# Performance work log

Measured on AMD Instinct MI355X. Metric: run time of the kernel, lower is better.

Reference implementation:

```python
import jax, jax.numpy as jnp
import numpy as np

C = 256
G = 32  # GroupNorm groups
EPS = 1e-6


def setup_inputs() -> dict:
    key = jax.random.key(0)
    ks = jax.random.split(key, 11)
    B, H, W = 4, 64, 64
    scale = 0.02
    return {
        "x": jax.random.normal(ks[0], (B, C, H, W), dtype=jnp.float32),
        "gn_scale": jnp.ones((C,), jnp.float32),
        "gn_bias": jnp.zeros((C,), jnp.float32),
        "wq": jax.random.normal(ks[1], (C, C), jnp.float32) * scale,
        "bq": jnp.zeros((C,), jnp.float32),
        "wk": jax.random.normal(ks[2], (C, C), jnp.float32) * scale,
        "bk": jnp.zeros((C,), jnp.float32),
        "wv": jax.random.normal(ks[3], (C, C), jnp.float32) * scale,
        "bv": jnp.zeros((C,), jnp.float32),
        "wp": jax.random.normal(ks[4], (C, C), jnp.float32) * scale,
        "bp": jnp.zeros((C,), jnp.float32),
    }


def _group_norm(x, scale, bias):
    b, c, h, w = x.shape
    xr = x.reshape(b, G, c // G, h, w)
    mu = jnp.mean(xr, axis=(2, 3, 4), keepdims=True)
    var = jnp.var(xr, axis=(2, 3, 4), keepdims=True)
    xn = ((xr - mu) * jax.lax.rsqrt(var + EPS)).reshape(b, c, h, w)
    return xn * scale[None, :, None, None] + bias[None, :, None, None]


def _conv1x1(x, w, bch):
    # 1x1 conv == channel-mixing matmul; w is (out_ch, in_ch)
    return jnp.einsum('bchw,dc->bdhw', x, w) + bch[None, :, None, None]


def reference(x, gn_scale, gn_bias, wq, bq, wk, bk, wv, bv, wp, bp):
    b, c, h, w = x.shape
    hn = _group_norm(x, gn_scale, gn_bias)
    q = _conv1x1(hn, wq, bq).reshape(b, c, h * w)  # (b,c,N)
    k = _conv1x1(hn, wk, bk).reshape(b, c, h * w)
    v = _conv1x1(hn, wv, bv).reshape(b, c, h * w)
    # attn[b,i,j] = softmax_j( q_i . k_j / sqrt(c) )
    attn = jax.nn.softmax(jnp.einsum('bci,bcj->bij', q, k) * (c ** -0.5), axis=-1)
    A = jnp.einsum('bcj,bij->bci', v, attn).reshape(b, c, h, w)
    return x + _conv1x1(A, wp, bp)
```

## Files before the change

### kernel.cpp

```cpp
#include <hip/hip_runtime.h>
#include <stdint.h>

#define Bn 4
#define Cn 256
#define Gn 32
#define Nn 4096
#define CGn 8

typedef unsigned short u16;
typedef __attribute__((ext_vector_type(8))) short short8;
typedef __attribute__((ext_vector_type(4))) short short4v;
typedef __attribute__((ext_vector_type(4))) float f32x4;
typedef __attribute__((ext_vector_type(16))) float f32x16;

__device__ __forceinline__ u16 f2bf(float x) {
  uint32_t u = __float_as_uint(x);
  u += 0x7fffu + ((u >> 16) & 1u);
  return (u16)(u >> 16);
}
__device__ __forceinline__ float b2f(u16 v) {
  return __uint_as_float(((uint32_t)v) << 16);
}

__device__ __forceinline__ void gl_lds16(const void* g, void* l) {
  __builtin_amdgcn_global_load_lds(
      (__attribute__((address_space(1))) void*)(uintptr_t)g,
      (__attribute__((address_space(3))) void*)(uintptr_t)l, 16, 0, 0);
}

__device__ __forceinline__ int sw512(int row, int cb) { return row * 512 + ((cb ^ (row & 7)) * 16); }

__global__ void k_cs(const float* __restrict__ wq, const float* __restrict__ wk,
                     const float* __restrict__ wv, const float* __restrict__ wp,
                     const float* __restrict__ bq, const float* __restrict__ bk,
                     const float* __restrict__ bv, const float* __restrict__ x,
                     u16* __restrict__ wqkv, u16* __restrict__ wpb,
                     float* __restrict__ bqkv, float* __restrict__ stats) {
  if (blockIdx.x < 256) {
    const float s = 0.09016844005556021f;
    int i = blockIdx.x * 256 + threadIdx.x;
    wqkv[i]          = f2bf(wq[i] * s);
    wqkv[i + 65536]  = f2bf(wk[i]);
    wqkv[i + 131072] = f2bf(wv[i]);
    wpb[i]           = f2bf(wp[i]);
    if (i < 256) { bqkv[i] = bq[i] * s; bqkv[i + 256] = bk[i]; bqkv[i + 512] = bv[i]; }
  } else {
    int blk = blockIdx.x - 256;
    int grp = blk >> 2, part = blk & 3;
    const float4* base = (const float4*)(x + (size_t)grp * (CGn * Nn) + part * 8192);
    float s = 0.f, s2 = 0.f;
    for (int i = threadIdx.x; i < 2048; i += 256) {
      float4 v = base[i];
      s  += v.x + v.y + v.z + v.w;
      s2 += v.x * v.x + v.y * v.y + v.z * v.z + v.w * v.w;
    }
#pragma unroll
    for (int m = 1; m < 64; m <<= 1) { s += __shfl_xor(s, m, 64); s2 += __shfl_xor(s2, m, 64); }
    __shared__ float ps[4], ps2[4];
    int w = threadIdx.x >> 6;
    if ((threadIdx.x & 63) == 0) { ps[w] = s; ps2[w] = s2; }
    __syncthreads();
    if (threadIdx.x == 0) {
      stats[grp * 8 + part * 2]     = ps[0] + ps[1] + ps[2] + ps[3];
      stats[grp * 8 + part * 2 + 1] = ps2[0] + ps2[1] + ps2[2] + ps2[3];
    }
  }
}

__global__ void k_apply(const float* __restrict__ x, const float* __restrict__ stats,
                        const float* __restrict__ gsc, const float* __restrict__ gbi,
                        u16* __restrict__ hnT) {
  __shared__ __align__(16) char smem[32768];
  __shared__ float smu[Gn], srs[Gn];
  int n0 = blockIdx.x * 64;
  int b = blockIdx.y;
  int tid = threadIdx.x;
  if (tid < Gn) {
    float S = 0.f, S2 = 0.f;
#pragma unroll
    for (int p = 0; p < 4; ++p) {
      S  += stats[(b * Gn + tid) * 8 + p * 2];
      S2 += stats[(b * Gn + tid) * 8 + p * 2 + 1];
    }
    const float inv = 1.f / (CGn * Nn);
    float mu = S * inv;
    float var = S2 * inv - mu * mu;
    smu[tid] = mu;
    srs[tid] = rsqrtf(var + 1e-6f);
  }
  __syncthreads();
  int nl = (tid & 15) * 4;
  int cbase = tid >> 4;
  for (int pass = 0; pass < 16; ++pass) {
    int c = pass * 16 + cbase;
    float4 v = *(const float4*)(x + (size_t)b * Cn * Nn + (size_t)c * Nn + n0 + nl);
    int g = c >> 3;
    float sc = gsc[c] * srs[g];
    float bi = gbi[c] - smu[g] * sc;
    float vals[4] = {v.x, v.y, v.z, v.w};
#pragma unroll
    for (int i = 0; i < 4; ++i) {
      int row = nl + i;
      int off = row * 512 + ((((c >> 3) + row) & 31) * 16) + (c & 7) * 2;
      *(u16*)(smem + off) = f2bf(vals[i] * sc + bi);
    }
  }
  __syncthreads();
#pragma unroll
  for (int p = 0; p < 8; ++p) {
    int idx = p * 256 + tid;
    int row = idx >> 5, pc = idx & 31;
    int gc = (pc - row) & 31;
    short8 v8 = *(const short8*)(smem + row * 512 + pc * 16);
    *(short8*)(hnT + ((size_t)b * Nn + n0 + row) * Cn + gc * 8) = v8;
  }
}

__global__ __launch_bounds__(256, 2)
void k_qkv(const u16* __restrict__ wqkv, const float* __restrict__ bqkv,
           const u16* __restrict__ hnT, u16* __restrict__ qT, u16* __restrict__ kT,
           u16* __restrict__ vv) {
  __shared__ __align__(16) char smem[65536];
  const int tid = threadIdx.x, lane = tid & 63, w = tid >> 6;
  const int quad = (lane >> 4) & 3, low = lane & 15;
  const int d0 = blockIdx.y * 64, b = blockIdx.z;
  const int n_base = blockIdx.x * 256;
  const int which = d0 >> 8;
  const int dl0 = d0 & 255;
  const u16* hb = hnT + (size_t)b * Nn * Cn;
  const int scol = lane & 31;

#define QKV_STAGE(bsel, nt)                                                     \
  {                                                                             \
    _Pragma("unroll") for (int s = 0; s < 8; ++s) {                             \
      int r = w * 16 + s * 2 + (lane >> 5);                                     \
      int gc = (scol - r) & 31;                                                 \
      gl_lds16(hb + (size_t)(n_base + (nt) * 64 + r) * Cn + gc * 8,             \
               smem + (bsel) * 32768 + (w * 16 + s * 2) * 512);                 \
    }                                                                           \
  }

  QKV_STAGE(0, 0);
  short8 af[8];
  {
    const u16* wrow = wqkv + (size_t)(d0 + w * 16 + low) * Cn + quad * 8;
#pragma unroll
    for (int kk = 0; kk < 8; ++kk) af[kk] = *(const short8*)(wrow + kk * 32);
  }
  float bias[4];
#pragma unroll
  for (int r = 0; r < 4; ++r) bias[r] = bqkv[d0 + w * 16 + quad * 4 + r];

  for (int nt = 0; nt < 4; ++nt) {
    if (nt < 3) {
      QKV_STAGE((nt + 1) & 1, nt + 1);
      asm volatile("s_waitcnt vmcnt(10)" ::: "memory");
    } else {
      asm volatile("s_waitcnt vmcnt(0)" ::: "memory");
    }
    asm volatile("s_barrier" ::: "memory");
    char* buf = smem + (nt & 1) * 32768;
    f32x4 acc[4] = {{0.f,0.f,0.f,0.f},{0.f,0.f,0.f,0.f},{0.f,0.f,0.f,0.f},{0.f,0.f,0.f,0.f}};
#pragma unroll
    for (int kk = 0; kk < 8; ++kk)
#pragma unroll
      for (int t = 0; t < 4; ++t) {
        int row = t * 16 + low;
        short8 bf = *(const short8*)(buf + row * 512 + (((kk * 4 + quad) + row) & 31) * 16);
        acc[t] = __builtin_amdgcn_mfma_f32_16x16x32_bf16(af[kk], bf, acc[t], 0, 0, 0);
      }
    asm volatile("s_barrier" ::: "memory");
    char* Q = buf + w * 8192;
    if (which == 2) {
#pragma unroll
      for (int t = 0; t < 4; ++t)
#pragma unroll
        for (int r = 0; r < 4; ++r)
          *(u16*)(Q + (quad * 4 + r) * 144 + t * 32 + low * 2) = f2bf(acc[t][r] + bias[r]);
#pragma unroll
      for (int s = 0; s < 2; ++s) {
        int slot = s * 64 + lane;
        int row = slot >> 3, ch = slot & 7;
        short8 v8 = *(const short8*)(Q + row * 144 + ch * 16);
        *(short8*)(vv + (size_t)b * Cn * Nn + (size_t)(dl0 + w * 16 + row) * Nn +
                   n_base + nt * 64 + ch * 8) = v8;
      }
    } else {
#pragma unroll
      for (int t = 0; t < 4; ++t) {
        short4v pk;
#pragma unroll
        for (int r = 0; r < 4; ++r) pk[r] = (short)f2bf(acc[t][r] + bias[r]);
        *(short4v*)(Q + (t * 16 + low) * 48 + quad * 8) = pk;
      }
      u16* dst = (which == 0 ? qT : kT) + (size_t)b * Nn * Cn;
#pragma unroll
      for (int s = 0; s < 2; ++s) {
        int slot = s * 64 + lane;
        int row = slot >> 1, half = slot & 1;
        short8 v8 = *(const short8*)(Q + row * 48 + half * 16);
        *(short8*)(dst + (size_t)(n_base + nt * 64 + row) * Cn + dl0 + w * 16 + half * 8) = v8;
      }
    }
  }
#undef QKV_STAGE
}

__device__ __forceinline__ void flash_stage(char* smem, int bsel, const u16* kTb,
                                            const u16* vb, int j0, int w, int lo,
                                            int kr, int vr, int vp) {
  char* ksb = smem + bsel * 32768;
  char* vsb = ksb + 16384;
#pragma unroll
  for (int s = 0; s < 4; ++s) {
    int j = kr + s * 2;
    int gc = (lo - j) & 31;
    gl_lds16(kTb + (size_t)(j0 + j) * Cn + gc * 8, ksb + (w * 8 + s * 2) * 512);
  }
#pragma unroll
  for (int s = 0; s < 4; ++s) {
    int c = vr + s * 16;
    int gc = (vp - c - (c >> 2)) & 3;
    gl_lds16(vb + (size_t)c * Nn + j0 + gc * 8, vsb + (w * 64 + s * 16) * 64);
  }
}

__global__ __launch_bounds__(256, 2)
void k_flash(const u16* __restrict__ qT, const u16* __restrict__ kT,
             const u16* __restrict__ vv, u16* __restrict__ Op0,
             u16* __restrict__ Op1, u16* __restrict__ Op2, u16* __restrict__ Op3,
             float* __restrict__ lrow) {
  __shared__ __align__(16) char smem[65536];
  const int tid = threadIdx.x, lane = tid & 63, w = tid >> 6;
  const int lo = lane & 31, hi = lane >> 5;
  const int i0 = blockIdx.x * 128;
  const int b = blockIdx.y, jh = blockIdx.z;
  const u16* qTb = qT + (size_t)b * Nn * Cn;
  const u16* kTb = kT + (size_t)b * Nn * Cn;
  const u16* vb  = vv + (size_t)b * Cn * Nn;
  const int u7 = lo + hi;
  const int u9 = lo + hi + (lo >> 2);
  const int kr = w * 8 + hi;
  const int vr = w * 64 + (lane >> 2);
  const int vp = lane & 3;

  flash_stage(smem, 0, kTb, vb, jh * 1024, w, lo, kr, vr, vp);

  short8 qf[16];
  {
    const u16* qrow = qTb + (size_t)(i0 + w * 32 + lo) * Cn + hi * 8;
#pragma unroll
    for (int ks = 0; ks < 16; ++ks) qf[ks] = *(const short8*)(qrow + ks * 16);
  }
  f32x16 Oa[8];
#pragma unroll
  for (int ct = 0; ct < 8; ++ct)
#pragma unroll
    for (int e = 0; e < 16; ++e) Oa[ct][e] = 0.f;
  float l_ = 0.f;

  for (int jt = 0; jt < 32; ++jt) {
    if (jt < 31) {
      flash_stage(smem, (jt + 1) & 1, kTb, vb, jh * 1024 + (jt + 1) * 32, w, lo, kr, vr, vp);
      asm volatile("s_waitcnt vmcnt(8)" ::: "memory");
    } else {
      asm volatile("s_waitcnt vmcnt(0)" ::: "memory");
    }
    asm volatile("s_barrier" ::: "memory");
    const char* ksb = smem + (jt & 1) * 32768;
    const char* vsb = ksb + 16384;

    f32x16 S0;
#pragma unroll
    for (int e = 0; e < 16; ++e) S0[e] = 0.f;
#pragma unroll
    for (int ks = 0; ks < 16; ++ks) {
      int ch = (ks * 2 + u7) & 31;
      short8 a0 = *(const short8*)(ksb + lo * 512 + ch * 16);
      S0 = __builtin_amdgcn_mfma_f32_32x32x16_bf16(a0, qf[ks], S0, 0, 0, 0);
    }
    uint32_t Pp[8];
#pragma unroll
    for (int g = 0; g < 8; ++g) {
      float p0 = __builtin_amdgcn_exp2f(S0[2 * g]);
      float p1 = __builtin_amdgcn_exp2f(S0[2 * g + 1]);
      l_ += p0 + p1;
      Pp[g] = ((uint32_t)f2bf(p1) << 16) | f2bf(p0);
    }
#pragma unroll
    for (int kst = 0; kst < 2; ++kst) {
      uint32_t a0 = Pp[4 * kst], a1 = Pp[4 * kst + 1];
      uint32_t b0 = Pp[4 * kst + 2], b1 = Pp[4 * kst + 3];
      uint32_t s0 = hi ? a0 : b0, s1 = hi ? a1 : b1;
      uint32_t r0 = (uint32_t)__shfl_xor((int)s0, 32, 64);
      uint32_t r1 = (uint32_t)__shfl_xor((int)s1, 32, 64);
      union { uint32_t u[4]; short8 s8; } pu;
      pu.u[0] = hi ? r0 : a0;
      pu.u[1] = hi ? r1 : a1;
      pu.u[2] = hi ? b0 : r0;
      pu.u[3] = hi ? b1 : r1;
      int ch = (kst * 2 + u9) & 3;
#pragma unroll
      for (int ct = 0; ct < 8; ++ct) {
        short8 vf = *(const short8*)(vsb + (ct * 32 + lo) * 64 + ch * 16);
        Oa[ct] = __builtin_amdgcn_mfma_f32_32x32x16_bf16(vf, pu.s8, Oa[ct], 0, 0, 0);
      }
    }
    asm volatile("s_barrier" ::: "memory");
  }

  l_ += __shfl_xor(l_, 32, 64);
  if (hi == 0)
    lrow[(size_t)jh * (Bn * Nn) + (size_t)b * Nn + i0 + w * 32 + lo] = l_;
  float invl = __builtin_amdgcn_rcpf(l_);
  __syncthreads();
#pragma unroll
  for (int ct = 0; ct < 8; ++ct)
#pragma unroll
    for (int g = 0; g < 4; ++g) {
      short4v pk;
#pragma unroll
      for (int r = 0; r < 4; ++r) pk[r] = (short)f2bf(Oa[ct][g * 4 + r] * invl);
      int chv = (ct * 4 + g + lo) & 31;
      *(short4v*)(smem + w * 16384 + lo * 512 + chv * 16 + hi * 8) = pk;
    }
  __syncthreads();
  u16* Opj = (jh == 0) ? Op0 : (jh == 1) ? Op1 : (jh == 2) ? Op2 : Op3;
  u16* Ob = Opj + ((size_t)b * Nn + i0 + w * 32) * (size_t)Cn;
#pragma unroll
  for (int s = 0; s < 16; ++s) {
    int rr = s * 2 + hi;
    short8 v8 = *(const short8*)(smem + w * 16384 + rr * 512 + lo * 16);
    int gc = (lo - rr) & 31;
    *(short8*)(Ob + (size_t)rr * Cn + gc * 8) = v8;
  }
}

__global__ void k_comb(const u16* __restrict__ O0, const u16* __restrict__ O1,
                       const u16* __restrict__ O2, const u16* __restrict__ O3,
                       const float* __restrict__ lrow, u16* __restrict__ OT) {
  int gid = blockIdx.x * 256 + threadIdx.x;
  int row = gid >> 6;
  int c4 = (gid & 63) << 2;
  float L = lrow[row] + lrow[Bn * Nn + row] + lrow[2 * Bn * Nn + row] + lrow[3 * Bn * Nn + row];
  float inv = __builtin_amdgcn_rcpf(L);
  size_t base = (size_t)row * Cn + c4;
  short4v a0 = *(const short4v*)(O0 + base);
  short4v a1 = *(const short4v*)(O1 + base);
  short4v a2 = *(const short4v*)(O2 + base);
  short4v a3 = *(const short4v*)(O3 + base);
  short4v o;
#pragma unroll
  for (int i = 0; i < 4; ++i)
    o[i] = (short)f2bf((b2f((u16)a0[i]) + b2f((u16)a1[i]) + b2f((u16)a2[i]) + b2f((u16)a3[i])) * inv);
  *(short4v*)(OT + base) = o;
}

__global__ __launch_bounds__(256, 2)
void k_proj(const u16* __restrict__ wpb, const float* __restrict__ bp,
            const u16* __restrict__ OT, const float* __restrict__ x,
            float* __restrict__ out) {
  __shared__ __align__(16) char smem[65536];
  int tid = threadIdx.x, lane = tid & 63, w = tid >> 6, quad = lane >> 4, low = lane & 15;
  int n0 = blockIdx.x * 64, d0 = blockIdx.y * 64, b = blockIdx.z;
  {
    int r0 = w * 16;
#pragma unroll
    for (int s = 0; s < 8; ++s) {
      int rs = r0 + s * 2;
      int r = rs + (lane >> 5);
      int cb = (lane & 31) ^ (r & 7);
      gl_lds16(wpb + (size_t)(d0 + r) * Cn + cb * 8, smem + rs * 512);
      gl_lds16(OT + ((size_t)b * Nn + n0 + r) * Cn + cb * 8, smem + 32768 + rs * 512);
    }
  }
  asm volatile("s_waitcnt vmcnt(0)" ::: "memory");
  __syncthreads();
  f32x4 acc[4] = {{0.f,0.f,0.f,0.f},{0.f,0.f,0.f,0.f},{0.f,0.f,0.f,0.f},{0.f,0.f,0.f,0.f}};
#pragma unroll
  for (int kk = 0; kk < 8; ++kk) {
    short8 af = *(const short8*)(smem + sw512(w * 16 + low, kk * 4 + quad));
#pragma unroll
    for (int t = 0; t < 4; ++t) {
      short8 bf = *(const short8*)(smem + 32768 + sw512(t * 16 + low, kk * 4 + quad));
      acc[t] = __builtin_amdgcn_mfma_f32_16x16x32_bf16(af, bf, acc[t], 0, 0, 0);
    }
  }
  int dloc = d0 + w * 16 + quad * 4;
#pragma unroll
  for (int t = 0; t < 4; ++t)
#pragma unroll
    for (int r = 0; r < 4; ++r) {
      size_t idx = (size_t)b * Cn * Nn + (size_t)(dloc + r) * Nn + n0 + t * 16 + low;
      out[idx] = x[idx] + acc[t][r] + bp[dloc + r];
    }
}

extern "C" void kernel_launch(void* const* d_in, const int* in_sizes, int n_in,
                              void* d_out, int out_size, void* d_ws, size_t ws_size,
                              hipStream_t stream) {
  const float* x   = (const float*)d_in[0];
  const float* gsc = (const float*)d_in[1];
  const float* gbi = (const float*)d_in[2];
  const float* wq  = (const float*)d_in[3];
  const float* bq  = (const float*)d_in[4];
  const float* wk  = (const float*)d_in[5];
  const float* bk  = (const float*)d_in[6];
  const float* wv  = (const float*)d_in[7];
  const float* bv  = (const float*)d_in[8];
  const float* wp  = (const float*)d_in[9];
  const float* bp  = (const float*)d_in[10];
  float* out = (float*)d_out;

  char* ws = (char*)d_ws;
  u16*   wqkv  = (u16*)(ws + 0);
  u16*   wpb   = (u16*)(ws + 393216);
  float* bqkv  = (float*)(ws + 524288);
  float* stats = (float*)(ws + 527360);
  float* lrow  = (float*)(ws + 532480);
  u16*   hnT   = (u16*)(ws + 1048576);
  u16*   qT    = (u16*)(ws + 9437184);
  u16*   kT    = (u16*)(ws + 17825792);
  u16*   vv    = (u16*)(ws + 26214400);
  u16*   Op1   = (u16*)(ws + 34603008);
  u16*   Op2   = (u16*)(ws + 42991616);
  u16*   Op3   = (u16*)(ws + 51380224);

  k_cs<<<768, 256, 0, stream>>>(wq, wk, wv, wp, bq, bk, bv, x, wqkv, wpb, bqkv, stats);
  k_apply<<<dim3(64, 4), 256, 0, stream>>>(x, stats, gsc, gbi, hnT);
  k_qkv<<<dim3(16, 12, 4), 256, 0, stream>>>(wqkv, bqkv, hnT, qT, kT, vv);
  k_flash<<<dim3(32, 4, 4), 256, 0, stream>>>(qT, kT, vv, hnT , Op1, Op2, Op3, lrow);
  k_comb<<<4096, 256, 0, stream>>>(hnT, Op1, Op2, Op3, lrow, qT );
  k_proj<<<dim3(64, 4, 4), 256, 0, stream>>>(wpb, bp, qT , x, out);
}
```

Baseline: 200.9 us.

## Use hardware bf16 pack conversion, permlane32 swap, and MFMA priority hints

Replaces the software round-to-nearest-even bf16 conversion with the gfx950 v_cvt_pk_bf16_f32 instruction in the QKV projection, flash softmax and output epilogue. Replaces the shfl_xor-and-select exchange of P fragments between wave halves with v_permlane32_swap_b32. Wraps the MFMA loops in s_setprio raises so waves issuing matrix ops are favored during scheduling. The aim is to cut VALU and LDS-permute overhead in the attention inner loop; the priority hints may or may not help interleaving across waves.

```diff
diff --git a/kernel.cpp b/kernel.cpp
--- a/kernel.cpp
+++ b/kernel.cpp
@@ -175,8 +175,14 @@
 #pragma unroll
       for (int t = 0; t < 4; ++t)
 #pragma unroll
-        for (int r = 0; r < 4; ++r)
-          *(u16*)(Q + (quad * 4 + r) * 144 + t * 32 + low * 2) = f2bf(acc[t][r] + bias[r]);
+        for (int rp = 0; rp < 2; ++rp) {
+          uint32_t wv2;
+          float f0 = acc[t][2 * rp] + bias[2 * rp];
+          float f1 = acc[t][2 * rp + 1] + bias[2 * rp + 1];
+          asm("v_cvt_pk_bf16_f32 %0, %1, %2" : "=v"(wv2) : "v"(f0), "v"(f1));
+          *(u16*)(Q + (quad * 4 + 2 * rp) * 144 + t * 32 + low * 2) = (u16)wv2;
+          *(u16*)(Q + (quad * 4 + 2 * rp + 1) * 144 + t * 32 + low * 2) = (u16)(wv2 >> 16);
+        }
 #pragma unroll
       for (int s = 0; s < 2; ++s) {
         int slot = s * 64 + lane;
@@ -188,10 +194,12 @@
     } else {
 #pragma unroll
       for (int t = 0; t < 4; ++t) {
-        short4v pk;
-#pragma unroll
-        for (int r = 0; r < 4; ++r) pk[r] = (short)f2bf(acc[t][r] + bias[r]);
-        *(short4v*)(Q + (t * 16 + low) * 48 + quad * 8) = pk;
+        union { uint32_t u[2]; short4v s; } pk;
+        float f0 = acc[t][0] + bias[0], f1 = acc[t][1] + bias[1];
+        float f2 = acc[t][2] + bias[2], f3 = acc[t][3] + bias[3];
+        asm("v_cvt_pk_bf16_f32 %0, %1, %2" : "=v"(pk.u[0]) : "v"(f0), "v"(f1));
+        asm("v_cvt_pk_bf16_f32 %0, %1, %2" : "=v"(pk.u[1]) : "v"(f2), "v"(f3));
+        *(short4v*)(Q + (t * 16 + low) * 48 + quad * 8) = pk.s;
       }
       u16* dst = (which == 0 ? qT : kT) + (size_t)b * Nn * Cn;
 #pragma unroll
@@ -273,38 +281,41 @@
     f32x16 S0;
 #pragma unroll
     for (int e = 0; e < 16; ++e) S0[e] = 0.f;
+    __builtin_amdgcn_s_setprio(1);
 #pragma unroll
     for (int ks = 0; ks < 16; ++ks) {
       int ch = (ks * 2 + u7) & 31;
       short8 a0 = *(const short8*)(ksb + lo * 512 + ch * 16);
       S0 = __builtin_amdgcn_mfma_f32_32x32x16_bf16(a0, qf[ks], S0, 0, 0, 0);
     }
+    __builtin_amdgcn_s_setprio(0);
     uint32_t Pp[8];
 #pragma unroll
     for (int g = 0; g < 8; ++g) {
       float p0 = __builtin_amdgcn_exp2f(S0[2 * g]);
       float p1 = __builtin_amdgcn_exp2f(S0[2 * g + 1]);
       l_ += p0 + p1;
-      Pp[g] = ((uint32_t)f2bf(p1) << 16) | f2bf(p0);
+      asm("v_cvt_pk_bf16_f32 %0, %1, %2" : "=v"(Pp[g]) : "v"(p0), "v"(p1));
     }
 #pragma unroll
     for (int kst = 0; kst < 2; ++kst) {
-      uint32_t a0 = Pp[4 * kst], a1 = Pp[4 * kst + 1];
-      uint32_t b0 = Pp[4 * kst + 2], b1 = Pp[4 * kst + 3];
-      uint32_t s0 = hi ? a0 : b0, s1 = hi ? a1 : b1;
-      uint32_t r0 = (uint32_t)__shfl_xor((int)s0, 32, 64);
-      uint32_t r1 = (uint32_t)__shfl_xor((int)s1, 32, 64);
+      uint32_t x0 = Pp[4 * kst], x1 = Pp[4 * kst + 1];
+      uint32_t y0 = Pp[4 * kst + 2], y1 = Pp[4 * kst + 3];
+      asm("v_permlane32_swap_b32 %0, %1" : "+v"(x0), "+v"(y0));
+      asm("v_permlane32_swap_b32 %0, %1" : "+v"(x1), "+v"(y1));
       union { uint32_t u[4]; short8 s8; } pu;
-      pu.u[0] = hi ? r0 : a0;
-      pu.u[1] = hi ? r1 : a1;
-      pu.u[2] = hi ? b0 : r0;
-      pu.u[3] = hi ? b1 : r1;
+      pu.u[0] = x0;
+      pu.u[1] = x1;
+      pu.u[2] = y0;
+      pu.u[3] = y1;
       int ch = (kst * 2 + u9) & 3;
+      __builtin_amdgcn_s_setprio(1);
 #pragma unroll
       for (int ct = 0; ct < 8; ++ct) {
         short8 vf = *(const short8*)(vsb + (ct * 32 + lo) * 64 + ch * 16);
         Oa[ct] = __builtin_amdgcn_mfma_f32_32x32x16_bf16(vf, pu.s8, Oa[ct], 0, 0, 0);
       }
+      __builtin_amdgcn_s_setprio(0);
     }
     asm volatile("s_barrier" ::: "memory");
   }
@@ -318,11 +329,13 @@
   for (int ct = 0; ct < 8; ++ct)
 #pragma unroll
     for (int g = 0; g < 4; ++g) {
-      short4v pk;
-#pragma unroll
-      for (int r = 0; r < 4; ++r) pk[r] = (short)f2bf(Oa[ct][g * 4 + r] * invl);
+      union { uint32_t u[2]; short4v s; } pk;
+      float f0 = Oa[ct][g * 4 + 0] * invl, f1 = Oa[ct][g * 4 + 1] * invl;
+      float f2 = Oa[ct][g * 4 + 2] * invl, f3 = Oa[ct][g * 4 + 3] * invl;
+      asm("v_cvt_pk_bf16_f32 %0, %1, %2" : "=v"(pk.u[0]) : "v"(f0), "v"(f1));
+      asm("v_cvt_pk_bf16_f32 %0, %1, %2" : "=v"(pk.u[1]) : "v"(f2), "v"(f3));
       int chv = (ct * 4 + g + lo) & 31;
-      *(short4v*)(smem + w * 16384 + lo * 512 + chv * 16 + hi * 8) = pk;
+      *(short4v*)(smem + w * 16384 + lo * 512 + chv * 16 + hi * 8) = pk.s;
     }
   __syncthreads();
   u16* Opj = (jh == 0) ? Op0 : (jh == 1) ? Op1 : (jh == 2) ? Op2 : Op3;
```

Measured after the change: 194.9 us. -3.0%, faster.
